# Kernel tuning notes

Measured on AMD Instinct MI355X. Metric: run time of the kernel, lower is better.

Reference implementation:

```python
import jax, jax.numpy as jnp
import numpy as np

B, S, T = 8192, 128, 64
OBS, LAT = 64, 128
ENC_H, ODE_H, DEC_H = 256, 256, 256
SUBSTEPS = 4  # fixed-step RK4 substeps per prediction interval (stands in for adaptive dopri5)


def _linear_params(key, fan_in, fan_out):
    k1, k2 = jax.random.split(key)
    bound = 1.0 / np.sqrt(fan_in)
    W = jax.random.uniform(k1, (fan_in, fan_out), jnp.float32, -bound, bound)
    b = jax.random.uniform(k2, (fan_out,), jnp.float32, -bound, bound)
    return W, b


def setup_inputs() -> dict:
    key = jax.random.key(0)
    ks = jax.random.split(key, 10)
    Wi2h, bi2h = _linear_params(ks[0], OBS + ENC_H, ENC_H)
    Wh2o, bh2o = _linear_params(ks[1], ENC_H, 2 * LAT)
    Wode1, bode1 = _linear_params(ks[2], LAT, ODE_H)
    Wode2, bode2 = _linear_params(ks[3], ODE_H, LAT)
    Wdec1, bdec1 = _linear_params(ks[4], LAT, DEC_H)
    Wdec2, bdec2 = _linear_params(ks[5], DEC_H, OBS)
    return {
        "observed_data": jax.random.normal(ks[6], (B, S, OBS), jnp.float32),
        "observed_times": jnp.sort(jax.random.uniform(ks[7], (S,), jnp.float32)),
        "prediction_times": jnp.arange(T, dtype=jnp.float32),
        "eps": jax.random.normal(ks[8], (B, LAT), jnp.float32),
        "Wi2h": Wi2h, "bi2h": bi2h, "Wh2o": Wh2o, "bh2o": bh2o,
        "Wode1": Wode1, "bode1": bode1, "Wode2": Wode2, "bode2": bode2,
        "Wdec1": Wdec1, "bdec1": bdec1, "Wdec2": Wdec2, "bdec2": bdec2,
    }


def reference(observed_data, observed_times, prediction_times, eps,
              Wi2h, bi2h, Wh2o, bh2o,
              Wode1, bode1, Wode2, bode2,
              Wdec1, bdec1, Wdec2, bdec2):
    b = observed_data.shape[0]
    latent = Wh2o.shape[1] // 2

    # --- Encoder: RNN over observed sequence, processed backwards ---
    h0 = jnp.zeros((b, Wi2h.shape[1]), observed_data.dtype)
    xs = observed_data[:, ::-1, :].transpose(1, 0, 2)  # [S, B, OBS], reversed time

    def cell(h, x):
        comb = jnp.concatenate([x, h], axis=1)  # [B, OBS+H]
        h_new = jnp.tanh(comb @ Wi2h + bi2h)
        return h_new, None

    h_final, _ = jax.lax.scan(cell, h0, xs)
    out = h_final @ Wh2o + bh2o  # [B, 2*LAT]
    z0_mean = out[:, :latent]
    z0_logvar = out[:, latent:]

    # --- Reparametrize ---
    z0 = z0_mean + eps * jnp.exp(0.5 * z0_logvar)

    # --- ODE integration (fixed-step RK4) ---
    def f(z):  # time-invariant ODE func: Linear -> tanh -> Linear
        return jnp.tanh(z @ Wode1 + bode1) @ Wode2 + bode2

    dts = jnp.diff(prediction_times) / SUBSTEPS  # [T-1]

    def interval(z, dt):
        def rk4(zc, _):
            k1 = f(zc)
            k2 = f(zc + 0.5 * dt * k1)
            k3 = f(zc + 0.5 * dt * k2)
            k4 = f(zc + dt * k3)
            return zc + (dt / 6.0) * (k1 + 2 * k2 + 2 * k3 + k4), None
        z_new, _ = jax.lax.scan(rk4, z, None, length=SUBSTEPS)
        return z_new, z_new

    _, traj = jax.lax.scan(interval, z0, dts)  # [T-1, B, LAT]
    z_traj = jnp.concatenate([z0[None], traj], axis=0)  # [T, B, LAT]

    # --- Decoder MLP ---
    hdec = jnp.maximum(z_traj @ Wdec1 + bdec1, 0.0)
    predicted_obs = hdec @ Wdec2 + bdec2  # [T, B, OBS]

    return predicted_obs, z0_mean, z0_logvar
```

## Files before the change

kernel.cpp:

```cpp
#include <hip/hip_runtime.h>
#include <math.h>

#define NTH 512
#define BT  32

#define MEAN_OFF 33554432u
#define LV_OFF   34603008u

__device__ __forceinline__ void gl_lds16(const float* g, float* l) {
  __builtin_amdgcn_global_load_lds(
      (const __attribute__((address_space(1))) void*)g,
      (__attribute__((address_space(3))) void*)l,
      16, 0, 0);
}

__device__ __forceinline__ void stage_async(const float* __restrict__ g,
                                            float* __restrict__ l, int tid) {
#pragma unroll
  for (int u = 0; u < 4; ++u)
    gl_lds16(g + u * 2048 + tid * 4, l + u * 2048 + tid * 4);
}

template<int SA>
__device__ __forceinline__ void g1_chunk(const float* __restrict__ A,
                                         const float* __restrict__ W,
                                         int cc, float (&acc)[8][2]) {
#pragma unroll 4
  for (int j4 = 0; j4 < 8; ++j4) {
    const int kk = j4 * 4;
    float4 a[8];
#pragma unroll
    for (int i = 0; i < 8; ++i)
      a[i] = *(const float4*)(A + i * SA + kk);
    float2 w[4];
#pragma unroll
    for (int j = 0; j < 4; ++j)
      w[j] = *(const float2*)(W + (kk + j) * 256 + cc);
#pragma unroll
    for (int i = 0; i < 8; ++i) {
      const float af[4] = {a[i].x, a[i].y, a[i].z, a[i].w};
#pragma unroll
      for (int j = 0; j < 4; ++j) {
        acc[i][0] = fmaf(af[j], w[j].x, acc[i][0]);
        acc[i][1] = fmaf(af[j], w[j].y, acc[i][1]);
      }
    }
  }
}

__device__ __forceinline__ void g2_chunk(const float* __restrict__ A,
                                         const float* __restrict__ W,
                                         int c2, float (&acc)[4][2]) {
#pragma unroll 4
  for (int j4 = 0; j4 < 16; ++j4) {
    const int kk = j4 * 4;
    float4 a[4];
#pragma unroll
    for (int i = 0; i < 4; ++i)
      a[i] = *(const float4*)(A + i * 256 + kk);
    float2 w[4];
#pragma unroll
    for (int j = 0; j < 4; ++j)
      w[j] = *(const float2*)(W + (kk + j) * 128 + c2);
#pragma unroll
    for (int i = 0; i < 4; ++i) {
      const float af[4] = {a[i].x, a[i].y, a[i].z, a[i].w};
#pragma unroll
      for (int j = 0; j < 4; ++j) {
        acc[i][0] = fmaf(af[j], w[j].x, acc[i][0]);
        acc[i][1] = fmaf(af[j], w[j].y, acc[i][1]);
      }
    }
  }
}

__device__ __forceinline__ void gd2_chunk(const float* __restrict__ A,
                                          const float* __restrict__ W,
                                          int cd, float (&acc)[4]) {
#pragma unroll 4
  for (int j4 = 0; j4 < 32; ++j4) {
    const int kk = j4 * 4;
    float4 a[4];
#pragma unroll
    for (int i = 0; i < 4; ++i)
      a[i] = *(const float4*)(A + i * 256 + kk);
    float w[4];
#pragma unroll
    for (int j = 0; j < 4; ++j)
      w[j] = W[(kk + j) * 64 + cd];
#pragma unroll
    for (int i = 0; i < 4; ++i) {
      const float af[4] = {a[i].x, a[i].y, a[i].z, a[i].w};
#pragma unroll
      for (int j = 0; j < 4; ++j)
        acc[i] = fmaf(af[j], w[j], acc[i]);
    }
  }
}

extern "C" __global__ void __launch_bounds__(NTH, 2)
latent_ode_fused(const float* __restrict__ obs,
                 const float* __restrict__ ptimes,
                 const float* __restrict__ eps,
                 const float* __restrict__ Wi2h, const float* __restrict__ bi2h,
                 const float* __restrict__ Wh2o, const float* __restrict__ bh2o,
                 const float* __restrict__ Wode1, const float* __restrict__ bode1,
                 const float* __restrict__ Wode2, const float* __restrict__ bode2,
                 const float* __restrict__ Wdec1, const float* __restrict__ bdec1,
                 const float* __restrict__ Wdec2, const float* __restrict__ bdec2,
                 float* __restrict__ out)
{
  __shared__ float smem[28672];
  float* const H     = smem;
  float* const ZC    = smem;
  float* const TMP   = smem + 4096;
  float* const XS    = smem + 8192;
  float* const WBUF0 = smem + 12288;
  float* const WBUF1 = smem + 20480;

  const int tid  = threadIdx.x;
  const int b0   = blockIdx.x * BT;
  const int wave = tid >> 6;
  const int lane = tid & 63;

  const int r1 = (wave >> 1) * 8;
  const int cc = (wave & 1) * 128 + lane * 2;
  const int r2 = wave * 4;
  const int c2 = lane * 2;
  const int rd = wave * 4;
  const int cd = lane;

  const float2 be  = *(const float2*)(bi2h + cc);
  const float2 bm  = *(const float2*)(bh2o + cc);
  const float2 bo1 = *(const float2*)(bode1 + cc);
  const float2 bo2 = *(const float2*)(bode2 + c2);
  const float2 bd1 = *(const float2*)(bdec1 + cc);
  const float  bd2 = bdec2[cd];

  for (int u = tid; u < 2048; u += NTH)
    *(float4*)(smem + u * 4) = make_float4(0.f, 0.f, 0.f, 0.f);

  {
    const int rr = tid >> 4, kp = (tid & 15) * 4;
    gl_lds16(obs + ((size_t)(b0 + rr) * 128 + 127) * 64 + kp, XS + 2048 + tid * 4);
    stage_async(Wi2h, WBUF0, tid);
  }

  float acc[8][2];
#pragma unroll
  for (int i = 0; i < 8; ++i) { acc[i][0] = be.x; acc[i][1] = be.y; }

#pragma unroll 1
  for (int it = 0; it < 128; ++it) {
    const int s = 127 - it;
    const float* xs_cur = XS + (s & 1) * 2048;
#pragma unroll 1
    for (int c = 0; c < 10; ++c) {
      __syncthreads();
      if (c == 0) {
        if (it > 0) {
#pragma unroll
          for (int i = 0; i < 8; ++i) {
            *(float2*)(H + (r1 + i) * 256 + cc) =
                make_float2(tanhf(acc[i][0]), tanhf(acc[i][1]));
            acc[i][0] = be.x; acc[i][1] = be.y;
          }
        }
        if (s > 0) {
          const int rr = tid >> 4, kp = (tid & 15) * 4;
          gl_lds16(obs + ((size_t)(b0 + rr) * 128 + (s - 1)) * 64 + kp,
                   XS + ((s - 1) & 1) * 2048 + tid * 4);
        }
      }
      const float* nw = (c < 9) ? (Wi2h + (size_t)(c + 1) * 8192)
                                : ((it < 127) ? Wi2h : Wh2o);
      stage_async(nw, (c & 1) ? WBUF0 : WBUF1, tid);
      const float* wc = (c & 1) ? WBUF1 : WBUF0;
      if (c < 2) g1_chunk<64>(xs_cur + r1 * 64 + 32 * c, wc, cc, acc);
      else       g1_chunk<256>(H + r1 * 256 + 32 * (c - 2), wc, cc, acc);
    }
  }

  __syncthreads();
#pragma unroll
  for (int i = 0; i < 8; ++i) {
    *(float2*)(H + (r1 + i) * 256 + cc) =
        make_float2(tanhf(acc[i][0]), tanhf(acc[i][1]));
    acc[i][0] = bm.x; acc[i][1] = bm.y;
  }
#pragma unroll 1
  for (int c = 0; c < 8; ++c) {
    __syncthreads();
    const float* nw = (c < 7) ? (Wh2o + (size_t)(c + 1) * 8192) : Wdec1;
    stage_async(nw, (c & 1) ? WBUF0 : WBUF1, tid);
    g1_chunk<256>(H + r1 * 256 + 32 * c, (c & 1) ? WBUF1 : WBUF0, cc, acc);
  }
  __syncthreads();
#pragma unroll
  for (int i = 0; i < 8; ++i)
    *(float2*)(TMP + (r1 + i) * 256 + cc) = make_float2(acc[i][0], acc[i][1]);
  __syncthreads();

  float z[4][2];
#pragma unroll
  for (int i = 0; i < 4; ++i) {
    const float2 m  = *(const float2*)(TMP + (r2 + i) * 256 + c2);
    const float2 lv = *(const float2*)(TMP + (r2 + i) * 256 + c2 + 128);
    const float2 e  = *(const float2*)(eps + (size_t)(b0 + r2 + i) * 128 + c2);
    *(float2*)(out + MEAN_OFF + (size_t)(b0 + r2 + i) * 128 + c2) = m;
    *(float2*)(out + LV_OFF   + (size_t)(b0 + r2 + i) * 128 + c2) = lv;
    z[i][0] = m.x + e.x * expf(0.5f * lv.x);
    z[i][1] = m.y + e.y * expf(0.5f * lv.y);
    *(float2*)(ZC + (r2 + i) * 128 + c2) = make_float2(z[i][0], z[i][1]);
  }

  auto decode = [&](int t, const float* nextW) {
    float a1[8][2];
#pragma unroll
    for (int i = 0; i < 8; ++i) { a1[i][0] = bd1.x; a1[i][1] = bd1.y; }
#pragma unroll 1
    for (int c = 0; c < 4; ++c) {
      __syncthreads();
      const float* nw = (c < 3) ? (Wdec1 + (size_t)(c + 1) * 8192) : Wdec2;
      stage_async(nw, (c & 1) ? WBUF0 : WBUF1, tid);
      g1_chunk<128>(ZC + r1 * 128 + 32 * c, (c & 1) ? WBUF1 : WBUF0, cc, a1);
    }
#pragma unroll
    for (int i = 0; i < 8; ++i)
      *(float2*)(TMP + (r1 + i) * 256 + cc) =
          make_float2(fmaxf(a1[i][0], 0.f), fmaxf(a1[i][1], 0.f));
    float a2[4];
#pragma unroll
    for (int i = 0; i < 4; ++i) a2[i] = bd2;
#pragma unroll 1
    for (int c = 0; c < 2; ++c) {
      __syncthreads();
      const float* nw = (c < 1) ? (Wdec2 + 8192) : nextW;
      stage_async(nw, (c & 1) ? WBUF0 : WBUF1, tid);
      gd2_chunk(TMP + rd * 256 + 128 * c, (c & 1) ? WBUF1 : WBUF0, cd, a2);
    }
#pragma unroll
    for (int i = 0; i < 4; ++i)
      out[(size_t)t * 524288 + (size_t)(b0 + rd + i) * 64 + cd] = a2[i];
  };

  auto feval = [&](const float* nextW, float (&f)[4][2]) {
    float a1[8][2];
#pragma unroll
    for (int i = 0; i < 8; ++i) { a1[i][0] = bo1.x; a1[i][1] = bo1.y; }
#pragma unroll 1
    for (int c = 0; c < 4; ++c) {
      __syncthreads();
      const float* nw = (c < 3) ? (Wode1 + (size_t)(c + 1) * 8192) : Wode2;
      stage_async(nw, (c & 1) ? WBUF0 : WBUF1, tid);
      g1_chunk<128>(ZC + r1 * 128 + 32 * c, (c & 1) ? WBUF1 : WBUF0, cc, a1);
    }
#pragma unroll
    for (int i = 0; i < 8; ++i)
      *(float2*)(TMP + (r1 + i) * 256 + cc) =
          make_float2(tanhf(a1[i][0]), tanhf(a1[i][1]));
    float a2[4][2];
#pragma unroll
    for (int i = 0; i < 4; ++i) { a2[i][0] = bo2.x; a2[i][1] = bo2.y; }
#pragma unroll 1
    for (int c = 0; c < 4; ++c) {
      __syncthreads();
      const float* nw = (c < 3) ? (Wode2 + (size_t)(c + 1) * 8192) : nextW;
      stage_async(nw, (c & 1) ? WBUF0 : WBUF1, tid);
      g2_chunk(TMP + r2 * 256 + 64 * c, (c & 1) ? WBUF1 : WBUF0, c2, a2);
    }
#pragma unroll
    for (int i = 0; i < 4; ++i) { f[i][0] = a2[i][0]; f[i][1] = a2[i][1]; }
  };

  decode(0, Wode1);

  float kacc[4][2];
#pragma unroll 1
  for (int t = 0; t < 63; ++t) {
    const float dt = (ptimes[t + 1] - ptimes[t]) * 0.25f;
#pragma unroll 1
    for (int ss = 0; ss < 4; ++ss) {
      float f[4][2];
      feval(Wode1, f);
      {
        const float h = 0.5f * dt;
#pragma unroll
        for (int i = 0; i < 4; ++i) {
          float2 v;
          kacc[i][0] = f[i][0]; v.x = fmaf(h, f[i][0], z[i][0]);
          kacc[i][1] = f[i][1]; v.y = fmaf(h, f[i][1], z[i][1]);
          *(float2*)(ZC + (r2 + i) * 128 + c2) = v;
        }
      }
      feval(Wode1, f);
      {
        const float h = 0.5f * dt;
#pragma unroll
        for (int i = 0; i < 4; ++i) {
          float2 v;
          kacc[i][0] = fmaf(2.f, f[i][0], kacc[i][0]); v.x = fmaf(h, f[i][0], z[i][0]);
          kacc[i][1] = fmaf(2.f, f[i][1], kacc[i][1]); v.y = fmaf(h, f[i][1], z[i][1]);
          *(float2*)(ZC + (r2 + i) * 128 + c2) = v;
        }
      }
      feval(Wode1, f);
      {
#pragma unroll
        for (int i = 0; i < 4; ++i) {
          float2 v;
          kacc[i][0] = fmaf(2.f, f[i][0], kacc[i][0]); v.x = fmaf(dt, f[i][0], z[i][0]);
          kacc[i][1] = fmaf(2.f, f[i][1], kacc[i][1]); v.y = fmaf(dt, f[i][1], z[i][1]);
          *(float2*)(ZC + (r2 + i) * 128 + c2) = v;
        }
      }
      feval((ss < 3) ? Wode1 : Wdec1, f);
      {
        const float h6 = dt * (1.0f / 6.0f);
#pragma unroll
        for (int i = 0; i < 4; ++i) {
          float2 v;
          z[i][0] = fmaf(h6, kacc[i][0] + f[i][0], z[i][0]); v.x = z[i][0];
          z[i][1] = fmaf(h6, kacc[i][1] + f[i][1], z[i][1]); v.y = z[i][1];
          *(float2*)(ZC + (r2 + i) * 128 + c2) = v;
        }
      }
    }
    decode(t + 1, Wode1);
  }
}

extern "C" void kernel_launch(void* const* d_in, const int* in_sizes, int n_in,
                              void* d_out, int out_size, void* d_ws, size_t ws_size,
                              hipStream_t stream) {
  const float* obs    = (const float*)d_in[0];
  const float* ptimes = (const float*)d_in[2];
  const float* eps    = (const float*)d_in[3];
  const float* Wi2h   = (const float*)d_in[4];
  const float* bi2h   = (const float*)d_in[5];
  const float* Wh2o   = (const float*)d_in[6];
  const float* bh2o   = (const float*)d_in[7];
  const float* Wode1  = (const float*)d_in[8];
  const float* bode1  = (const float*)d_in[9];
  const float* Wode2  = (const float*)d_in[10];
  const float* bode2  = (const float*)d_in[11];
  const float* Wdec1  = (const float*)d_in[12];
  const float* bdec1  = (const float*)d_in[13];
  const float* Wdec2  = (const float*)d_in[14];
  const float* bdec2  = (const float*)d_in[15];

  latent_ode_fused<<<dim3(8192 / BT), dim3(NTH), 0, stream>>>(
      obs, ptimes, eps, Wi2h, bi2h, Wh2o, bh2o,
      Wode1, bode1, Wode2, bode2, Wdec1, bdec1, Wdec2, bdec2,
      (float*)d_out);
}
```

Baseline: 25.34 ms.

## Triple-buffer weight staging with prefetch distance two and per-block slab rotation

In the ODE and decoder phases, weight chunk staging moves from double to triple buffering in LDS with a prefetch distance of two. Full __syncthreads barriers are replaced by an s_waitcnt vmcnt(4) plus s_barrier, so one chunk's async loads can stay in flight across the barrier. Slab order inside each staging call is rotated per block group to spread L2 and HBM accesses across blocks. LDS use grows from 112KB to 144KB per block, which may stop two 512-thread blocks fitting per CU, and the hand-written waitcnt depends on an exact count of outstanding loads.

```diff
diff --git a/kernel.cpp b/kernel.cpp
--- a/kernel.cpp
+++ b/kernel.cpp
@@ -14,11 +14,18 @@
       16, 0, 0);
 }
 
-__device__ __forceinline__ void stage_async(const float* __restrict__ g,
-                                            float* __restrict__ l, int tid) {
-#pragma unroll
-  for (int u = 0; u < 4; ++u)
-    gl_lds16(g + u * 2048 + tid * 4, l + u * 2048 + tid * 4);
+__device__ __forceinline__ void stage_async_rot(const float* __restrict__ g,
+                                                float* __restrict__ l,
+                                                int wave, int lane, int rot) {
+#pragma unroll
+  for (int u = 0; u < 4; ++u) {
+    const int slab = (wave + u * 8 + rot) & 31;
+    gl_lds16(g + slab * 256 + lane * 4, l + slab * 256 + lane * 4);
+  }
+}
+
+__device__ __forceinline__ void wait_barrier_v4() {
+  asm volatile("s_waitcnt vmcnt(4) lgkmcnt(0)\n\ts_barrier" ::: "memory");
 }
 
 template<int SA>
@@ -110,18 +117,20 @@
                  const float* __restrict__ Wdec2, const float* __restrict__ bdec2,
                  float* __restrict__ out)
 {
-  __shared__ float smem[28672];
+  __shared__ float smem[36864];
   float* const H     = smem;
   float* const ZC    = smem;
   float* const TMP   = smem + 4096;
   float* const XS    = smem + 8192;
-  float* const WBUF0 = smem + 12288;
-  float* const WBUF1 = smem + 20480;
+  float* const WB    = smem + 12288;
+  float* const WBUF0 = WB;
+  float* const WBUF1 = WB + 8192;
 
   const int tid  = threadIdx.x;
   const int b0   = blockIdx.x * BT;
   const int wave = tid >> 6;
   const int lane = tid & 63;
+  const int rot  = (blockIdx.x >> 3) & 31;
 
   const int r1 = (wave >> 1) * 8;
   const int cc = (wave & 1) * 128 + lane * 2;
@@ -143,7 +152,7 @@
   {
     const int rr = tid >> 4, kp = (tid & 15) * 4;
     gl_lds16(obs + ((size_t)(b0 + rr) * 128 + 127) * 64 + kp, XS + 2048 + tid * 4);
-    stage_async(Wi2h, WBUF0, tid);
+    stage_async_rot(Wi2h, WBUF0, wave, lane, rot);
   }
 
   float acc[8][2];
@@ -174,7 +183,7 @@
       }
       const float* nw = (c < 9) ? (Wi2h + (size_t)(c + 1) * 8192)
                                 : ((it < 127) ? Wi2h : Wh2o);
-      stage_async(nw, (c & 1) ? WBUF0 : WBUF1, tid);
+      stage_async_rot(nw, (c & 1) ? WBUF0 : WBUF1, wave, lane, rot);
       const float* wc = (c & 1) ? WBUF1 : WBUF0;
       if (c < 2) g1_chunk<64>(xs_cur + r1 * 64 + 32 * c, wc, cc, acc);
       else       g1_chunk<256>(H + r1 * 256 + 32 * (c - 2), wc, cc, acc);
@@ -192,10 +201,11 @@
   for (int c = 0; c < 8; ++c) {
     __syncthreads();
     const float* nw = (c < 7) ? (Wh2o + (size_t)(c + 1) * 8192) : Wdec1;
-    stage_async(nw, (c & 1) ? WBUF0 : WBUF1, tid);
+    stage_async_rot(nw, (c & 1) ? WBUF0 : WBUF1, wave, lane, rot);
     g1_chunk<256>(H + r1 * 256 + 32 * c, (c & 1) ? WBUF1 : WBUF0, cc, acc);
   }
   __syncthreads();
+  stage_async_rot(Wdec1 + 8192, WBUF1, wave, lane, rot);
 #pragma unroll
   for (int i = 0; i < 8; ++i)
     *(float2*)(TMP + (r1 + i) * 256 + cc) = make_float2(acc[i][0], acc[i][1]);
@@ -214,16 +224,21 @@
     *(float2*)(ZC + (r2 + i) * 128 + c2) = make_float2(z[i][0], z[i][1]);
   }
 
-  auto decode = [&](int t, const float* nextW) {
+  int cb = 0;
+
+  auto decode = [&](int t, const float* n0, const float* n1) {
     float a1[8][2];
 #pragma unroll
     for (int i = 0; i < 8; ++i) { a1[i][0] = bd1.x; a1[i][1] = bd1.y; }
 #pragma unroll 1
-    for (int c = 0; c < 4; ++c) {
-      __syncthreads();
-      const float* nw = (c < 3) ? (Wdec1 + (size_t)(c + 1) * 8192) : Wdec2;
-      stage_async(nw, (c & 1) ? WBUF0 : WBUF1, tid);
-      g1_chunk<128>(ZC + r1 * 128 + 32 * c, (c & 1) ? WBUF1 : WBUF0, cc, a1);
+    for (int b = 0; b < 4; ++b) {
+      wait_barrier_v4();
+      const float* p = (b < 2) ? (Wdec1 + (size_t)(b + 2) * 8192)
+                               : (Wdec2 + (size_t)(b - 2) * 8192);
+      int nb = cb + 2; if (nb >= 3) nb -= 3;
+      stage_async_rot(p, WB + nb * 8192, wave, lane, rot);
+      g1_chunk<128>(ZC + r1 * 128 + 32 * b, WB + cb * 8192, cc, a1);
+      cb = (cb == 2) ? 0 : cb + 1;
     }
 #pragma unroll
     for (int i = 0; i < 8; ++i)
@@ -233,27 +248,32 @@
 #pragma unroll
     for (int i = 0; i < 4; ++i) a2[i] = bd2;
 #pragma unroll 1
-    for (int c = 0; c < 2; ++c) {
-      __syncthreads();
-      const float* nw = (c < 1) ? (Wdec2 + 8192) : nextW;
-      stage_async(nw, (c & 1) ? WBUF0 : WBUF1, tid);
-      gd2_chunk(TMP + rd * 256 + 128 * c, (c & 1) ? WBUF1 : WBUF0, cd, a2);
+    for (int b = 0; b < 2; ++b) {
+      wait_barrier_v4();
+      const float* p = b ? n1 : n0;
+      int nb = cb + 2; if (nb >= 3) nb -= 3;
+      if (p) stage_async_rot(p, WB + nb * 8192, wave, lane, rot);
+      gd2_chunk(TMP + rd * 256 + 128 * b, WB + cb * 8192, cd, a2);
+      cb = (cb == 2) ? 0 : cb + 1;
     }
 #pragma unroll
     for (int i = 0; i < 4; ++i)
       out[(size_t)t * 524288 + (size_t)(b0 + rd + i) * 64 + cd] = a2[i];
   };
 
-  auto feval = [&](const float* nextW, float (&f)[4][2]) {
+  auto feval = [&](const float* n0, const float* n1, float (&f)[4][2]) {
     float a1[8][2];
 #pragma unroll
     for (int i = 0; i < 8; ++i) { a1[i][0] = bo1.x; a1[i][1] = bo1.y; }
 #pragma unroll 1
-    for (int c = 0; c < 4; ++c) {
-      __syncthreads();
-      const float* nw = (c < 3) ? (Wode1 + (size_t)(c + 1) * 8192) : Wode2;
-      stage_async(nw, (c & 1) ? WBUF0 : WBUF1, tid);
-      g1_chunk<128>(ZC + r1 * 128 + 32 * c, (c & 1) ? WBUF1 : WBUF0, cc, a1);
+    for (int b = 0; b < 4; ++b) {
+      wait_barrier_v4();
+      const float* p = (b < 2) ? (Wode1 + (size_t)(b + 2) * 8192)
+                               : (Wode2 + (size_t)(b - 2) * 8192);
+      int nb = cb + 2; if (nb >= 3) nb -= 3;
+      stage_async_rot(p, WB + nb * 8192, wave, lane, rot);
+      g1_chunk<128>(ZC + r1 * 128 + 32 * b, WB + cb * 8192, cc, a1);
+      cb = (cb == 2) ? 0 : cb + 1;
     }
 #pragma unroll
     for (int i = 0; i < 8; ++i)
@@ -263,17 +283,20 @@
 #pragma unroll
     for (int i = 0; i < 4; ++i) { a2[i][0] = bo2.x; a2[i][1] = bo2.y; }
 #pragma unroll 1
-    for (int c = 0; c < 4; ++c) {
-      __syncthreads();
-      const float* nw = (c < 3) ? (Wode2 + (size_t)(c + 1) * 8192) : nextW;
-      stage_async(nw, (c & 1) ? WBUF0 : WBUF1, tid);
-      g2_chunk(TMP + r2 * 256 + 64 * c, (c & 1) ? WBUF1 : WBUF0, c2, a2);
+    for (int b = 0; b < 4; ++b) {
+      wait_barrier_v4();
+      const float* p = (b < 2) ? (Wode2 + (size_t)(b + 2) * 8192)
+                               : ((b == 2) ? n0 : n1);
+      int nb = cb + 2; if (nb >= 3) nb -= 3;
+      stage_async_rot(p, WB + nb * 8192, wave, lane, rot);
+      g2_chunk(TMP + r2 * 256 + 64 * b, WB + cb * 8192, c2, a2);
+      cb = (cb == 2) ? 0 : cb + 1;
     }
 #pragma unroll
     for (int i = 0; i < 4; ++i) { f[i][0] = a2[i][0]; f[i][1] = a2[i][1]; }
   };
 
-  decode(0, Wode1);
+  decode(0, Wode1, Wode1 + 8192);
 
   float kacc[4][2];
 #pragma unroll 1
@@ -282,7 +305,7 @@
 #pragma unroll 1
     for (int ss = 0; ss < 4; ++ss) {
       float f[4][2];
-      feval(Wode1, f);
+      feval(Wode1, Wode1 + 8192, f);
       {
         const float h = 0.5f * dt;
 #pragma unroll
@@ -293,7 +316,7 @@
           *(float2*)(ZC + (r2 + i) * 128 + c2) = v;
         }
       }
-      feval(Wode1, f);
+      feval(Wode1, Wode1 + 8192, f);
       {
         const float h = 0.5f * dt;
 #pragma unroll
@@ -304,7 +327,7 @@
           *(float2*)(ZC + (r2 + i) * 128 + c2) = v;
         }
       }
-      feval(Wode1, f);
+      feval(Wode1, Wode1 + 8192, f);
       {
 #pragma unroll
         for (int i = 0; i < 4; ++i) {
@@ -314,7 +337,8 @@
           *(float2*)(ZC + (r2 + i) * 128 + c2) = v;
         }
       }
-      feval((ss < 3) ? Wode1 : Wdec1, f);
+      if (ss < 3) feval(Wode1, Wode1 + 8192, f);
+      else        feval(Wdec1, Wdec1 + 8192, f);
       {
         const float h6 = dt * (1.0f / 6.0f);
 #pragma unroll
@@ -326,7 +350,8 @@
         }
       }
     }
-    decode(t + 1, Wode1);
+    if (t < 62) decode(t + 1, Wode1, Wode1 + 8192);
+    else        decode(t + 1, nullptr, nullptr);
   }
 }
 
```

Result: slower. 26.23 ms (+3.5%).
